# Kernel optimization log

Hardware: AMD Instinct MI355X
Metric: run time of the kernel (lower is better)

## Reference

```python
import jax, jax.numpy as jnp
import numpy as np

B, T, C, H = 4, 2048, 768, 12
D = C // H

def setup_inputs() -> dict:
    key = jax.random.key(0)
    ks = jax.random.split(key, 8)
    s = 1.0 / np.sqrt(C)
    return {
        "x":  jax.random.normal(ks[0], (B, T, C), dtype=jnp.float32),
        "Wq": jax.random.normal(ks[1], (C, C), dtype=jnp.float32) * s,
        "bq": jax.random.normal(ks[2], (C,), dtype=jnp.float32) * 0.02,
        "Wk": jax.random.normal(ks[3], (C, C), dtype=jnp.float32) * s,
        "bk": jax.random.normal(ks[4], (C,), dtype=jnp.float32) * 0.02,
        "Wv": jax.random.normal(ks[5], (C, C), dtype=jnp.float32) * s,
        "bv": jax.random.normal(ks[6], (C,), dtype=jnp.float32) * 0.02,
        "Wp": jax.random.normal(ks[7], (C, C), dtype=jnp.float32) * s,
    }

def reference(x, Wq, bq, Wk, bk, Wv, bv, Wp):
    # Linear projections (torch Linear: y = x @ W.T + b)
    q = x @ Wq.T + bq
    k = x @ Wk.T + bk
    v = x @ Wv.T + bv
    # [B,T,C] -> [B,H,T,D]
    q = q.reshape(B, T, H, D).transpose(0, 2, 1, 3)
    k = k.reshape(B, T, H, D).transpose(0, 2, 1, 3)
    v = v.reshape(B, T, H, D).transpose(0, 2, 1, 3)
    scale = 1.0 / np.sqrt(D).astype(np.float32)
    scores = jnp.einsum('bhqd,bhkd->bhqk', q, k) * scale  # [B,H,T,T]
    attn = jax.nn.softmax(scores, axis=-1)  # no mask in original module
    out = jnp.einsum('bhqk,bhkd->bhqd', attn, v)
    out = out.transpose(0, 2, 1, 3).reshape(B, T, C)
    return out @ Wp.T  # proj has bias=False
```

## Files before the change

### kernel.cpp

```cpp
#include <hip/hip_runtime.h>
#include <hip/hip_bf16.h>
#include <cmath>

constexpr int B  = 4;
constexpr int T  = 2048;
constexpr int C  = 768;
constexpr int H  = 12;
constexpr int Dh = 64;
constexpr int M  = B * T;
constexpr int NQKV = 3 * C;
constexpr int WS2  = C * C;

typedef short bf16x8 __attribute__((ext_vector_type(8)));
typedef short bf16x4 __attribute__((ext_vector_type(4)));
typedef float f32x4  __attribute__((ext_vector_type(4)));

__device__ inline short f2bf(float f) {
    unsigned u = __float_as_uint(f);
    u += 0x7fffu + ((u >> 16) & 1u);
    return (short)(u >> 16);
}

__device__ inline unsigned pk_bf16(float a, float b) {
    __hip_bfloat162 h = __float22bfloat162_rn(float2{a, b});
    return *(unsigned*)&h;
}

typedef const __attribute__((address_space(1))) unsigned GU;
typedef __attribute__((address_space(3))) unsigned LU;
__device__ inline void async_copy16(const void* g, void* l) {
    __builtin_amdgcn_global_load_lds((GU*)g, (LU*)l, 16, 0, 0);
}

constexpr size_t XE = (size_t)M * C;
constexpr size_t CV_TOTAL = XE + 4 * (size_t)WS2;

__global__ __launch_bounds__(256)
void convert_all(const float* __restrict__ x,  const float* __restrict__ Wq,
                 const float* __restrict__ Wk, const float* __restrict__ Wv,
                 const float* __restrict__ Wp,
                 short* __restrict__ xb, short* __restrict__ Wqkv,
                 short* __restrict__ Wpb) {
    size_t i = ((size_t)blockIdx.x * 256 + threadIdx.x) * 4;
    const float* src; short* dst; size_t off;
    if (i < XE)                        { src = x;  dst = xb;            off = i; }
    else if (i < XE + WS2)             { src = Wq; dst = Wqkv;          off = i - XE; }
    else if (i < XE + 2 * (size_t)WS2) { src = Wk; dst = Wqkv + WS2;    off = i - XE - WS2; }
    else if (i < XE + 3 * (size_t)WS2) { src = Wv; dst = Wqkv + 2 * WS2; off = i - XE - 2 * (size_t)WS2; }
    else                               { src = Wp; dst = Wpb;           off = i - XE - 3 * (size_t)WS2; }
    float4 v = *(const float4*)(src + off);
    bf16x4 o; o[0] = f2bf(v.x); o[1] = f2bf(v.y); o[2] = f2bf(v.z); o[3] = f2bf(v.w);
    *(bf16x4*)(dst + off) = o;
}

constexpr int BM = 128;

template<int BN_, int WMW, int WNW, int OUT_BF16>
__global__ __launch_bounds__(256)
void gemm_bt(const short* __restrict__ A, const short* __restrict__ W,
             const float* __restrict__ bias0, const float* __restrict__ bias1,
             const float* __restrict__ bias2,
             void* __restrict__ Yv, int Ndim, int Kdim) {
    constexpr int MT  = BM / WMW / 16;
    constexpr int NT  = BN_ / WNW / 16;
    constexpr int NCH = (BM + BN_) / 16;

    __shared__ short As[2][BM * 32];
    __shared__ short Bs[2][BN_ * 32];

    const int tid  = threadIdx.x;
    const int wave = tid >> 6;
    const int lane = tid & 63;
    const int li   = lane & 15;
    const int quad = lane >> 4;
    const int wm   = wave % WMW;
    const int wn   = wave / WMW;
    const int m0   = blockIdx.y * BM;
    const int n0   = blockIdx.x * BN_;

    f32x4 acc[MT][NT];
    #pragma unroll
    for (int i = 0; i < MT; ++i)
        #pragma unroll
        for (int j = 0; j < NT; ++j)
            acc[i][j] = (f32x4){0.f, 0.f, 0.f, 0.f};

    const int lrow = lane >> 2;
    const int lkof = (lane & 3) * 8;

    auto stage = [&](int kk, int pbuf) {
        #pragma unroll
        for (int ii = 0; ii < NCH / 4; ++ii) {
            int c = ii * 4 + wave;
            if (c < BM / 16)
                async_copy16(A + (size_t)(m0 + c * 16 + lrow) * Kdim + kk + lkof,
                             &As[pbuf][c * 512]);
            else
                async_copy16(W + (size_t)(n0 + (c - BM / 16) * 16 + lrow) * Kdim + kk + lkof,
                             &Bs[pbuf][(c - BM / 16) * 512]);
        }
    };

    stage(0, 0);

    int pi = 0;
    for (int k0 = 0; k0 < Kdim; k0 += 32, pi ^= 1) {
        __syncthreads();
        if (k0 + 32 < Kdim) stage(k0 + 32, pi ^ 1);

        bf16x8 af[MT], bfr[NT];
        #pragma unroll
        for (int t = 0; t < MT; ++t)
            af[t] = *(const bf16x8*)&As[pi][(wm * MT * 16 + t * 16 + li) * 32 + quad * 8];
        #pragma unroll
        for (int t = 0; t < NT; ++t)
            bfr[t] = *(const bf16x8*)&Bs[pi][(wn * NT * 16 + t * 16 + li) * 32 + quad * 8];
        #pragma unroll
        for (int i = 0; i < MT; ++i)
            #pragma unroll
            for (int j = 0; j < NT; ++j)
                acc[i][j] = __builtin_amdgcn_mfma_f32_16x16x32_bf16(
                    af[i], bfr[j], acc[i][j], 0, 0, 0);
    }

    float bb[NT];
    #pragma unroll
    for (int nt = 0; nt < NT; ++nt) bb[nt] = 0.f;
    if (bias0) {
        int s = n0 / C;
        const float* bp = (s == 0) ? bias0 : ((s == 1) ? bias1 : bias2);
        int nb = n0 % C;
        #pragma unroll
        for (int nt = 0; nt < NT; ++nt)
            bb[nt] = bp[nb + wn * NT * 16 + nt * 16 + li];
    }

    #pragma unroll
    for (int mt = 0; mt < MT; ++mt)
        #pragma unroll
        for (int nt = 0; nt < NT; ++nt)
            #pragma unroll
            for (int r = 0; r < 4; ++r) {
                int row = m0 + wm * MT * 16 + mt * 16 + quad * 4 + r;
                int col = n0 + wn * NT * 16 + nt * 16 + li;
                float v = acc[mt][nt][r] + bb[nt];
                if constexpr (OUT_BF16)
                    ((short*)Yv)[(size_t)row * Ndim + col] = f2bf(v);
                else
                    ((float*)Yv)[(size_t)row * Ndim + col] = v;
            }
}

constexpr int QT   = 128;
constexpr int KTT  = 64;
constexpr int LSTR = 72;
constexpr int PSTR = 72;
constexpr int QS   = NQKV;
constexpr float SOFT_SCALE = 0.18033688011112042f;

__global__ __launch_bounds__(256)
void attn_fwd(const short* __restrict__ QKV, short* __restrict__ O) {
    __shared__ short Ks[KTT * LSTR];
    __shared__ short Vt[Dh * LSTR];
    __shared__ short Ps[4 * 32 * PSTR];

    const int tid  = threadIdx.x;
    const int wave = tid >> 6;
    const int lane = tid & 63;
    const int li   = lane & 15;
    const int quad = lane >> 4;
    const int b    = blockIdx.z;
    const int h    = blockIdx.y;
    const int qw   = blockIdx.x * QT + wave * 32;

    const short* Qg = QKV + (size_t)(b * T) * QS + h * Dh;
    const short* Kg = QKV + (size_t)(b * T) * QS + C + h * Dh;
    const short* Vg = QKV + (size_t)(b * T) * QS + 2 * C + h * Dh;

    bf16x8 qf[2][2];
    #pragma unroll
    for (int qb = 0; qb < 2; ++qb)
        #pragma unroll
        for (int dh = 0; dh < 2; ++dh)
            qf[qb][dh] = *(const bf16x8*)(Qg + (size_t)(qw + qb * 16 + li) * QS
                                             + dh * 32 + quad * 8);

    bf16x8 ones;
    #pragma unroll
    for (int i = 0; i < 8; ++i) ones[i] = (short)0x3F80;

    f32x4 oacc[2][4];
    #pragma unroll
    for (int qb = 0; qb < 2; ++qb)
        #pragma unroll
        for (int db = 0; db < 4; ++db)
            oacc[qb][db] = (f32x4){0.f, 0.f, 0.f, 0.f};
    f32x4 lacc[2] = {(f32x4){0.f, 0.f, 0.f, 0.f}, (f32x4){0.f, 0.f, 0.f, 0.f}};

    const int ktok = tid >> 3;
    const int kch  = tid & 7;
    const int vd2  = (tid & 31) * 2;
    const int vg   = tid >> 5;

    int4 kpre[2];
    unsigned vpre[8];
    kpre[0] = *(const int4*)(Kg + (size_t)(ktok)      * QS + kch * 8);
    kpre[1] = *(const int4*)(Kg + (size_t)(ktok + 32) * QS + kch * 8);
    #pragma unroll
    for (int t2 = 0; t2 < 8; ++t2)
        vpre[t2] = *(const unsigned*)(Vg + (size_t)(vg * 8 + t2) * QS + vd2);

    for (int kt = 0; kt < T; kt += KTT) {
        __syncthreads();

        *(int4*)&Ks[ktok * LSTR + kch * 8]        = kpre[0];
        *(int4*)&Ks[(ktok + 32) * LSTR + kch * 8] = kpre[1];
        {
            unsigned lo[4], hi[4];
            #pragma unroll
            for (int j = 0; j < 4; ++j) {
                lo[j] = __builtin_amdgcn_perm(vpre[2 * j + 1], vpre[2 * j], 0x05040100u);
                hi[j] = __builtin_amdgcn_perm(vpre[2 * j + 1], vpre[2 * j], 0x07060302u);
            }
            *(int4*)&Vt[vd2 * LSTR + vg * 8]       = make_int4(lo[0], lo[1], lo[2], lo[3]);
            *(int4*)&Vt[(vd2 + 1) * LSTR + vg * 8] = make_int4(hi[0], hi[1], hi[2], hi[3]);
        }
        __syncthreads();

        if (kt + KTT < T) {
            const size_t nb = kt + KTT;
            kpre[0] = *(const int4*)(Kg + (nb + ktok)      * QS + kch * 8);
            kpre[1] = *(const int4*)(Kg + (nb + ktok + 32) * QS + kch * 8);
            #pragma unroll
            for (int t2 = 0; t2 < 8; ++t2)
                vpre[t2] = *(const unsigned*)(Vg + (nb + vg * 8 + t2) * QS + vd2);
        }

        f32x4 st[2][4];
        #pragma unroll
        for (int kb = 0; kb < 4; ++kb) {
            bf16x8 kf0 = *(const bf16x8*)&Ks[(kb * 16 + li) * LSTR + quad * 8];
            bf16x8 kf1 = *(const bf16x8*)&Ks[(kb * 16 + li) * LSTR + 32 + quad * 8];
            #pragma unroll
            for (int qb = 0; qb < 2; ++qb) {
                f32x4 a = (f32x4){0.f, 0.f, 0.f, 0.f};
                a = __builtin_amdgcn_mfma_f32_16x16x32_bf16(kf0, qf[qb][0], a, 0, 0, 0);
                a = __builtin_amdgcn_mfma_f32_16x16x32_bf16(kf1, qf[qb][1], a, 0, 0, 0);
                st[qb][kb] = a;
            }
        }

        #pragma unroll
        for (int qb = 0; qb < 2; ++qb)
            #pragma unroll
            for (int kb = 0; kb < 4; ++kb) {
                float p0 = __builtin_amdgcn_exp2f(st[qb][kb][0] * SOFT_SCALE);
                float p1 = __builtin_amdgcn_exp2f(st[qb][kb][1] * SOFT_SCALE);
                float p2 = __builtin_amdgcn_exp2f(st[qb][kb][2] * SOFT_SCALE);
                float p3 = __builtin_amdgcn_exp2f(st[qb][kb][3] * SOFT_SCALE);
                uint2 w; w.x = pk_bf16(p0, p1); w.y = pk_bf16(p2, p3);
                *(uint2*)&Ps[(wave * 32 + qb * 16 + li) * PSTR + kb * 16 + quad * 4] = w;
            }
        __asm__ volatile("s_waitcnt lgkmcnt(0)" ::: "memory");

        #pragma unroll
        for (int kq = 0; kq < 2; ++kq) {
            bf16x8 pf[2];
            #pragma unroll
            for (int qb = 0; qb < 2; ++qb) {
                pf[qb] = *(const bf16x8*)&Ps[(wave * 32 + qb * 16 + li) * PSTR
                                             + kq * 32 + quad * 8];
                lacc[qb] = __builtin_amdgcn_mfma_f32_16x16x32_bf16(
                    pf[qb], ones, lacc[qb], 0, 0, 0);
            }
            #pragma unroll
            for (int db = 0; db < 4; ++db) {
                bf16x8 vf = *(const bf16x8*)&Vt[(db * 16 + li) * LSTR + kq * 32 + quad * 8];
                #pragma unroll
                for (int qb = 0; qb < 2; ++qb)
                    oacc[qb][db] = __builtin_amdgcn_mfma_f32_16x16x32_bf16(
                        pf[qb], vf, oacc[qb][db], 0, 0, 0);
            }
        }
    }

    #pragma unroll
    for (int qb = 0; qb < 2; ++qb)
        #pragma unroll
        for (int r = 0; r < 4; ++r) {
            float inv = 1.0f / lacc[qb][r];
            short* op = O + (size_t)(b * T + qw + qb * 16 + quad * 4 + r) * C
                          + h * Dh + li;
            #pragma unroll
            for (int db = 0; db < 4; ++db)
                op[db * 16] = f2bf(oacc[qb][db][r] * inv);
        }
}

extern "C" void kernel_launch(void* const* d_in, const int* in_sizes, int n_in,
                              void* d_out, int out_size, void* d_ws, size_t ws_size,
                              hipStream_t stream) {
    (void)in_sizes; (void)n_in; (void)out_size; (void)ws_size;

    const float* x  = (const float*)d_in[0];
    const float* Wq = (const float*)d_in[1];
    const float* bq = (const float*)d_in[2];
    const float* Wk = (const float*)d_in[3];
    const float* bk = (const float*)d_in[4];
    const float* Wv = (const float*)d_in[5];
    const float* bv = (const float*)d_in[6];
    const float* Wp = (const float*)d_in[7];
    float* out = (float*)d_out;

    short* xb    = (short*)d_ws;
    short* Wqkv  = xb + (size_t)M * C;
    short* Wpb   = Wqkv + 3 * (size_t)WS2;
    short* QKVb  = Wpb + (size_t)WS2;
    short* AOb   = QKVb + (size_t)M * NQKV;

    convert_all<<<dim3(CV_TOTAL / 1024), 256, 0, stream>>>(
        x, Wq, Wk, Wv, Wp, xb, Wqkv, Wpb);

    gemm_bt<128, 2, 2, 1><<<dim3(NQKV / 128, M / BM), 256, 0, stream>>>(
        xb, Wqkv, bq, bk, bv, QKVb, NQKV, C);

    attn_fwd<<<dim3(T / QT, H, B), 256, 0, stream>>>(QKVb, AOb);

    gemm_bt<64, 4, 1, 0><<<dim3(C / 64, M / BM), 256, 0, stream>>>(
        AOb, Wpb, nullptr, nullptr, nullptr, out, C, C);
}
```

Before: 246.5 us.

## Split attention over two key halves and combine partials in a reduce kernel

```diff
diff --git a/kernel.cpp b/kernel.cpp
--- a/kernel.cpp
+++ b/kernel.cpp
@@ -151,17 +151,20 @@
             }
 }
 
-constexpr int QT   = 128;
-constexpr int KTT  = 64;
-constexpr int LSTR = 72;
-constexpr int PSTR = 72;
-constexpr int QS   = NQKV;
+constexpr int QT    = 128;
+constexpr int KTT   = 32;
+constexpr int KHALF = T / 2;
+constexpr int KSTR  = 72;
+constexpr int VSTR  = 40;
+constexpr int PSTR  = 40;
+constexpr int QS    = NQKV;
 constexpr float SOFT_SCALE = 0.18033688011112042f;
 
 __global__ __launch_bounds__(256)
-void attn_fwd(const short* __restrict__ QKV, short* __restrict__ O) {
-    __shared__ short Ks[KTT * LSTR];
-    __shared__ short Vt[Dh * LSTR];
+void attn_fwd(const short* __restrict__ QKV, float* __restrict__ Opart,
+              float* __restrict__ Lpart) {
+    __shared__ short Ks[KTT * KSTR];
+    __shared__ short Vt[Dh * VSTR];
     __shared__ short Ps[4 * 32 * PSTR];
 
     const int tid  = threadIdx.x;
@@ -169,9 +172,11 @@
     const int lane = tid & 63;
     const int li   = lane & 15;
     const int quad = lane >> 4;
-    const int b    = blockIdx.z;
+    const int half = blockIdx.z & 1;
+    const int b    = blockIdx.z >> 1;
     const int h    = blockIdx.y;
     const int qw   = blockIdx.x * QT + wave * 32;
+    const int kt0  = half * KHALF;
 
     const short* Qg = QKV + (size_t)(b * T) * QS + h * Dh;
     const short* Kg = QKV + (size_t)(b * T) * QS + C + h * Dh;
@@ -202,45 +207,40 @@
     const int vd2  = (tid & 31) * 2;
     const int vg   = tid >> 5;
 
-    int4 kpre[2];
-    unsigned vpre[8];
-    kpre[0] = *(const int4*)(Kg + (size_t)(ktok)      * QS + kch * 8);
-    kpre[1] = *(const int4*)(Kg + (size_t)(ktok + 32) * QS + kch * 8);
-    #pragma unroll
-    for (int t2 = 0; t2 < 8; ++t2)
-        vpre[t2] = *(const unsigned*)(Vg + (size_t)(vg * 8 + t2) * QS + vd2);
-
-    for (int kt = 0; kt < T; kt += KTT) {
+    int4 kpre;
+    unsigned vpre[4];
+    kpre = *(const int4*)(Kg + (size_t)(kt0 + ktok) * QS + kch * 8);
+    #pragma unroll
+    for (int t2 = 0; t2 < 4; ++t2)
+        vpre[t2] = *(const unsigned*)(Vg + (size_t)(kt0 + vg * 4 + t2) * QS + vd2);
+
+    for (int kt = kt0; kt < kt0 + KHALF; kt += KTT) {
         __syncthreads();
 
-        *(int4*)&Ks[ktok * LSTR + kch * 8]        = kpre[0];
-        *(int4*)&Ks[(ktok + 32) * LSTR + kch * 8] = kpre[1];
+        *(int4*)&Ks[ktok * KSTR + kch * 8] = kpre;
         {
-            unsigned lo[4], hi[4];
-            #pragma unroll
-            for (int j = 0; j < 4; ++j) {
-                lo[j] = __builtin_amdgcn_perm(vpre[2 * j + 1], vpre[2 * j], 0x05040100u);
-                hi[j] = __builtin_amdgcn_perm(vpre[2 * j + 1], vpre[2 * j], 0x07060302u);
-            }
-            *(int4*)&Vt[vd2 * LSTR + vg * 8]       = make_int4(lo[0], lo[1], lo[2], lo[3]);
-            *(int4*)&Vt[(vd2 + 1) * LSTR + vg * 8] = make_int4(hi[0], hi[1], hi[2], hi[3]);
+            unsigned lo0 = __builtin_amdgcn_perm(vpre[1], vpre[0], 0x05040100u);
+            unsigned lo1 = __builtin_amdgcn_perm(vpre[3], vpre[2], 0x05040100u);
+            unsigned hi0 = __builtin_amdgcn_perm(vpre[1], vpre[0], 0x07060302u);
+            unsigned hi1 = __builtin_amdgcn_perm(vpre[3], vpre[2], 0x07060302u);
+            *(uint2*)&Vt[vd2 * VSTR + vg * 4]       = make_uint2(lo0, lo1);
+            *(uint2*)&Vt[(vd2 + 1) * VSTR + vg * 4] = make_uint2(hi0, hi1);
         }
         __syncthreads();
 
-        if (kt + KTT < T) {
+        if (kt + KTT < kt0 + KHALF) {
             const size_t nb = kt + KTT;
-            kpre[0] = *(const int4*)(Kg + (nb + ktok)      * QS + kch * 8);
-            kpre[1] = *(const int4*)(Kg + (nb + ktok + 32) * QS + kch * 8);
-            #pragma unroll
-            for (int t2 = 0; t2 < 8; ++t2)
-                vpre[t2] = *(const unsigned*)(Vg + (nb + vg * 8 + t2) * QS + vd2);
-        }
-
-        f32x4 st[2][4];
-        #pragma unroll
-        for (int kb = 0; kb < 4; ++kb) {
-            bf16x8 kf0 = *(const bf16x8*)&Ks[(kb * 16 + li) * LSTR + quad * 8];
-            bf16x8 kf1 = *(const bf16x8*)&Ks[(kb * 16 + li) * LSTR + 32 + quad * 8];
+            kpre = *(const int4*)(Kg + (nb + ktok) * QS + kch * 8);
+            #pragma unroll
+            for (int t2 = 0; t2 < 4; ++t2)
+                vpre[t2] = *(const unsigned*)(Vg + (nb + vg * 4 + t2) * QS + vd2);
+        }
+
+        f32x4 st[2][2];
+        #pragma unroll
+        for (int kb = 0; kb < 2; ++kb) {
+            bf16x8 kf0 = *(const bf16x8*)&Ks[(kb * 16 + li) * KSTR + quad * 8];
+            bf16x8 kf1 = *(const bf16x8*)&Ks[(kb * 16 + li) * KSTR + 32 + quad * 8];
             #pragma unroll
             for (int qb = 0; qb < 2; ++qb) {
                 f32x4 a = (f32x4){0.f, 0.f, 0.f, 0.f};
@@ -253,7 +253,7 @@
         #pragma unroll
         for (int qb = 0; qb < 2; ++qb)
             #pragma unroll
-            for (int kb = 0; kb < 4; ++kb) {
+            for (int kb = 0; kb < 2; ++kb) {
                 float p0 = __builtin_amdgcn_exp2f(st[qb][kb][0] * SOFT_SCALE);
                 float p1 = __builtin_amdgcn_exp2f(st[qb][kb][1] * SOFT_SCALE);
                 float p2 = __builtin_amdgcn_exp2f(st[qb][kb][2] * SOFT_SCALE);
@@ -263,38 +263,60 @@
             }
         __asm__ volatile("s_waitcnt lgkmcnt(0)" ::: "memory");
 
-        #pragma unroll
-        for (int kq = 0; kq < 2; ++kq) {
-            bf16x8 pf[2];
-            #pragma unroll
-            for (int qb = 0; qb < 2; ++qb) {
-                pf[qb] = *(const bf16x8*)&Ps[(wave * 32 + qb * 16 + li) * PSTR
-                                             + kq * 32 + quad * 8];
-                lacc[qb] = __builtin_amdgcn_mfma_f32_16x16x32_bf16(
-                    pf[qb], ones, lacc[qb], 0, 0, 0);
-            }
-            #pragma unroll
-            for (int db = 0; db < 4; ++db) {
-                bf16x8 vf = *(const bf16x8*)&Vt[(db * 16 + li) * LSTR + kq * 32 + quad * 8];
-                #pragma unroll
-                for (int qb = 0; qb < 2; ++qb)
-                    oacc[qb][db] = __builtin_amdgcn_mfma_f32_16x16x32_bf16(
-                        pf[qb], vf, oacc[qb][db], 0, 0, 0);
-            }
+        bf16x8 pf[2];
+        #pragma unroll
+        for (int qb = 0; qb < 2; ++qb) {
+            pf[qb] = *(const bf16x8*)&Ps[(wave * 32 + qb * 16 + li) * PSTR + quad * 8];
+            lacc[qb] = __builtin_amdgcn_mfma_f32_16x16x32_bf16(
+                pf[qb], ones, lacc[qb], 0, 0, 0);
+        }
+        #pragma unroll
+        for (int db = 0; db < 4; ++db) {
+            bf16x8 vf = *(const bf16x8*)&Vt[(db * 16 + li) * VSTR + quad * 8];
+            #pragma unroll
+            for (int qb = 0; qb < 2; ++qb)
+                oacc[qb][db] = __builtin_amdgcn_mfma_f32_16x16x32_bf16(
+                    pf[qb], vf, oacc[qb][db], 0, 0, 0);
         }
     }
 
+    float* Ob = Opart + (size_t)half * M * C;
     #pragma unroll
     for (int qb = 0; qb < 2; ++qb)
         #pragma unroll
         for (int r = 0; r < 4; ++r) {
-            float inv = 1.0f / lacc[qb][r];
-            short* op = O + (size_t)(b * T + qw + qb * 16 + quad * 4 + r) * C
-                          + h * Dh + li;
+            int row = qw + qb * 16 + quad * 4 + r;
+            float* op = Ob + ((size_t)(b * T) + row) * C + h * Dh + li;
             #pragma unroll
             for (int db = 0; db < 4; ++db)
-                op[db * 16] = f2bf(oacc[qb][db][r] * inv);
-        }
+                op[db * 16] = oacc[qb][db][r];
+            if (li == 0)
+                Lpart[(size_t)half * M * H + ((size_t)(b * T) + row) * H + h]
+                    = lacc[qb][r];
+        }
+}
+
+__global__ __launch_bounds__(256)
+void attn_reduce(const float* __restrict__ Op, const float* __restrict__ Lp,
+                 short* __restrict__ AO) {
+    int i = (blockIdx.x * 256 + threadIdx.x) * 8;
+    int row = i / C;
+    int col = i % C;
+    int h = col >> 6;
+    float l = Lp[(size_t)row * H + h] + Lp[(size_t)M * H + (size_t)row * H + h];
+    float inv = 1.0f / l;
+    const float* p0 = Op + i;
+    const float* p1 = Op + (size_t)M * C + i;
+    float4 a0 = *(const float4*)(p0);
+    float4 a1 = *(const float4*)(p0 + 4);
+    float4 b0 = *(const float4*)(p1);
+    float4 b1 = *(const float4*)(p1 + 4);
+    bf16x8 o;
+    o[0] = f2bf((a0.x + b0.x) * inv); o[1] = f2bf((a0.y + b0.y) * inv);
+    o[2] = f2bf((a0.z + b0.z) * inv); o[3] = f2bf((a0.w + b0.w) * inv);
+    o[4] = f2bf((a1.x + b1.x) * inv); o[5] = f2bf((a1.y + b1.y) * inv);
+    o[6] = f2bf((a1.z + b1.z) * inv); o[7] = f2bf((a1.w + b1.w) * inv);
+    *(bf16x8*)(AO + i) = o;
 }
 
 extern "C" void kernel_launch(void* const* d_in, const int* in_sizes, int n_in,
@@ -313,10 +335,12 @@
     float* out = (float*)d_out;
 
     short* xb    = (short*)d_ws;
-    short* Wqkv  = xb + (size_t)M * C;
+    short* Wqkv  = xb + XE;
     short* Wpb   = Wqkv + 3 * (size_t)WS2;
     short* QKVb  = Wpb + (size_t)WS2;
-    short* AOb   = QKVb + (size_t)M * NQKV;
+    float* Opart = (float*)(QKVb + (size_t)M * NQKV);
+    float* Lpart = (float*)Wqkv;
+    short* AOb   = xb;
 
     convert_all<<<dim3(CV_TOTAL / 1024), 256, 0, stream>>>(
         x, Wq, Wk, Wv, Wp, xb, Wqkv, Wpb);
@@ -324,7 +348,9 @@
     gemm_bt<128, 2, 2, 1><<<dim3(NQKV / 128, M / BM), 256, 0, stream>>>(
         xb, Wqkv, bq, bk, bv, QKVb, NQKV, C);
 
-    attn_fwd<<<dim3(T / QT, H, B), 256, 0, stream>>>(QKVb, AOb);
+    attn_fwd<<<dim3(T / QT, H, B * 2), 256, 0, stream>>>(QKVb, Opart, Lpart);
+
+    attn_reduce<<<dim3((M * C) / 2048), 256, 0, stream>>>(Opart, Lpart, AOb);
 
     gemm_bt<64, 4, 1, 0><<<dim3(C / 64, M / BM), 256, 0, stream>>>(
         AOb, Wpb, nullptr, nullptr, nullptr, out, C, C);
```

Result: no change. 250.1 us (+1.5%).
